# Optimization experiments

Hardware: AMD Instinct MI355X
Metric: run time of the kernel (lower is better)

Reference implementation:

```python
import jax, jax.numpy as jnp
import numpy as np

B, T, V, E = 32, 12, 1024, 64
G = 32           # graph_emb
DAY, WEEK = 288, 7
ALPHA = 0.3      # LeakyReLU slope


def setup_inputs() -> dict:
    key = jax.random.key(0)
    ks = jax.random.split(key, 10)
    return {
        "inputs": jax.random.normal(ks[0], (B, T, V, E), dtype=jnp.float32),
        "n_route": jax.random.randint(ks[1], (B, V), 0, V),
        "s_week": jax.random.randint(ks[2], (B, T), 0, WEEK),
        "s_day": jax.random.randint(ks[3], (B, T), 0, DAY),
        "srpe": jax.random.normal(ks[4], (V, G, E), dtype=jnp.float32) * 0.05,
        "sape": jax.random.normal(ks[5], (V, T, E), dtype=jnp.float32) * 0.05,
        "dow_emb": jax.random.normal(ks[6], (WEEK, V, E), dtype=jnp.float32) * 0.05,
        "tod_emb": jax.random.normal(ks[7], (DAY, V, E), dtype=jnp.float32) * 0.05,
        "connect_weight": jax.random.normal(ks[8], (T, V, 3 * E, E), dtype=jnp.float32) * 0.05,
        "connect_bias": jnp.zeros((T, V, E), dtype=jnp.float32),
    }


def reference(inputs, n_route, s_week, s_day, srpe, sape, dow_emb, tod_emb,
              connect_weight, connect_bias):
    # relation scores: per-channel node-node affinity, relu'd. [V, V, E]
    relation_pos = jnp.einsum('vge,gie->vie', srpe,
                              jnp.transpose(srpe, (1, 0, 2)))
    relation_pos = jax.nn.relu(relation_pos)
    # per-channel graph mixing: contract over source node g. [B, T, V, E]
    x_rel_emb = jnp.einsum('vge,btge->btve', relation_pos, inputs)
    # spatial absolute position embedding gather: [B, V, T, E] -> [B, T, V, E]
    pos_emb = jnp.transpose(sape[n_route], (0, 2, 1, 3))
    # time embeddings: [B, T, V, E]
    time_emb = dow_emb[s_week] + tod_emb[s_day]
    # concat along feature dim -> [B, T, V, 3E]
    x_list = jnp.concatenate([x_rel_emb, pos_emb, time_emb], axis=-1)
    # distinct (3E x E) weight per (timestep, node): batched small matmul
    y = jnp.einsum('btgf,tgfe->btge', x_list, connect_weight) + connect_bias
    return jnp.where(y > 0, y, ALPHA * y)
```

## Files before the change

kernel.cpp:

```cpp
#include <hip/hip_runtime.h>
#include <stdint.h>

#define Bdim 32
#define Tdim 12
#define Vdim 1024
#define Edim 64
#define Gdim 32
#define BT   384

typedef __attribute__((ext_vector_type(8))) short bf16x8;
typedef __attribute__((ext_vector_type(4))) float f32x4;

__device__ __forceinline__ uint pk2(float a, float b) {
    uint r;
    asm("v_cvt_pk_bf16_f32 %0, %1, %2" : "=v"(r) : "v"(a), "v"(b));
    return r;
}
__device__ __forceinline__ ushort f2bf(float f) {
    return (ushort)(pk2(f, f) & 0xffffu);
}

__global__ __launch_bounds__(256) void k_xpose(const float* __restrict__ in,
                                               ushort* __restrict__ Xbf) {
    __shared__ float tile[64][68];
    const int bt = blockIdx.x >> 4;
    const int i0 = (blockIdx.x & 15) << 6;
    const int r  = threadIdx.x >> 2;
    const int q  = threadIdx.x & 3;
    const float* src = in + ((size_t)(bt * Vdim) + i0 + r) * Edim + q * 16;
#pragma unroll
    for (int k = 0; k < 4; ++k)
        *(float4*)&tile[r][q * 16 + 4 * k] = *(const float4*)(src + 4 * k);
    __syncthreads();
    const int e  = r;
    const int ib = q * 16;
    uint4 s0, s1;
    s0.x = pk2(tile[ib + 0][e],  tile[ib + 1][e]);
    s0.y = pk2(tile[ib + 2][e],  tile[ib + 3][e]);
    s0.z = pk2(tile[ib + 4][e],  tile[ib + 5][e]);
    s0.w = pk2(tile[ib + 6][e],  tile[ib + 7][e]);
    s1.x = pk2(tile[ib + 8][e],  tile[ib + 9][e]);
    s1.y = pk2(tile[ib + 10][e], tile[ib + 11][e]);
    s1.z = pk2(tile[ib + 12][e], tile[ib + 13][e]);
    s1.w = pk2(tile[ib + 14][e], tile[ib + 15][e]);
    ushort* dst = Xbf + ((size_t)(e * BT) + bt) * Vdim + i0 + ib;
    *(uint4*)dst = s0;
    *(uint4*)(dst + 8) = s1;
}

__global__ __launch_bounds__(256) void k_se(const float* __restrict__ srpe,
                                            ushort* __restrict__ Se) {
    __shared__ float t2[256][65];
    const int tid = threadIdx.x;
    const int v0 = blockIdx.x * 8;
#pragma unroll
    for (int c = 0; c < 16; ++c) {
        int f = (c * 256 + tid) * 4;
        int vg = f >> 6;
        int e4 = f & 63;
        *(float4*)&t2[vg][e4] = *(const float4*)(srpe + (size_t)v0 * Gdim * Edim + f);
    }
    __syncthreads();
    const int e = tid & 63;
#pragma unroll
    for (int h = 0; h < 2; ++h) {
        const int vv = (tid >> 6) * 2 + h;
        uint4 o[2];
#pragma unroll
        for (int c = 0; c < 2; ++c) {
            o[c].x = pk2(t2[vv * 32 + c * 16 + 0][e],  t2[vv * 32 + c * 16 + 1][e]);
            o[c].y = pk2(t2[vv * 32 + c * 16 + 2][e],  t2[vv * 32 + c * 16 + 3][e]);
            o[c].z = pk2(t2[vv * 32 + c * 16 + 4][e],  t2[vv * 32 + c * 16 + 5][e]);
            o[c].w = pk2(t2[vv * 32 + c * 16 + 6][e],  t2[vv * 32 + c * 16 + 7][e]);
        }
        uint4 o2[2];
#pragma unroll
        for (int c = 0; c < 2; ++c) {
            o2[c].x = pk2(t2[vv * 32 + c * 16 + 8][e],  t2[vv * 32 + c * 16 + 9][e]);
            o2[c].y = pk2(t2[vv * 32 + c * 16 + 10][e], t2[vv * 32 + c * 16 + 11][e]);
            o2[c].z = pk2(t2[vv * 32 + c * 16 + 12][e], t2[vv * 32 + c * 16 + 13][e]);
            o2[c].w = pk2(t2[vv * 32 + c * 16 + 14][e], t2[vv * 32 + c * 16 + 15][e]);
        }
        ushort* dst = Se + ((size_t)(e * Vdim) + v0 + vv) * Gdim;
        *(uint4*)(dst + 0)  = o[0];
        *(uint4*)(dst + 8)  = o2[0];
        *(uint4*)(dst + 16) = o[1];
        *(uint4*)(dst + 24) = o2[1];
    }
}

__global__ __launch_bounds__(256, 2) void k_relmix_mfma(const ushort* __restrict__ Xbf,
                                                        const ushort* __restrict__ Se,
                                                        ushort* __restrict__ xrel) {
    __shared__ __align__(16) ushort A_s[3][192 * 32];
    __shared__ __align__(16) ushort Si_s[3][32 * 32];
    __shared__ __align__(16) ushort R_s[2][128 * 40];

    const int tid = threadIdx.x;
    const int l = tid & 63;
    const int w = tid >> 6;
    const int wm = w >> 1;
    const int wn = w & 1;

    const int raw = blockIdx.x;
    const int wg  = (raw & 7) * 128 + (raw >> 3);
    const int e   = wg >> 4;
    const int btT = (wg >> 3) & 1;
    const int vT  = wg & 7;
    const int bt0 = btT * 192;
    const int v0  = vT * 128;

    const int lr  = l >> 2;
    const int lc  = ((l & 3) ^ (lr & 3)) * 8;

    const ushort* gA  = Xbf + ((size_t)(e * BT + bt0)) * Vdim;
    const ushort* gSi = Se + (size_t)e * Vdim * Gdim;

    bf16x8 svF[2];
    {
        const ushort* gSv = Se + ((size_t)e * Vdim + v0) * Gdim;
#pragma unroll
        for (int k = 0; k < 2; ++k) {
            const int vloc = (2 * w + k) * 16 + (l & 15);
            svF[k] = *(const bf16x8*)(gSv + (size_t)vloc * Gdim + (l >> 4) * 8);
        }
    }
    __builtin_amdgcn_sched_barrier(0);

    if (w < 2)
        __builtin_amdgcn_global_load_lds(gSi + (size_t)(0 + w * 16 + lr) * Gdim + lc,
                                         &Si_s[0][w * 512], 16, 0, 0);
#pragma unroll
    for (int c = 0; c < 3; ++c) {
        int chunk = w * 3 + c;
        __builtin_amdgcn_global_load_lds(gA + (size_t)(chunk * 16 + lr) * Vdim + 0 + lc,
                                         &A_s[0][chunk * 512], 16, 0, 0);
    }
    if (w < 2)
        __builtin_amdgcn_global_load_lds(gSi + (size_t)(32 + w * 16 + lr) * Gdim + lc,
                                         &Si_s[1][w * 512], 16, 0, 0);
#pragma unroll
    for (int c = 0; c < 3; ++c) {
        int chunk = w * 3 + c;
        __builtin_amdgcn_global_load_lds(gA + (size_t)(chunk * 16 + lr) * Vdim + 32 + lc,
                                         &A_s[1][chunk * 512], 16, 0, 0);
    }
    asm volatile("s_waitcnt vmcnt(3)" ::: "memory");
    __builtin_amdgcn_sched_barrier(0);
    __builtin_amdgcn_s_barrier();
    __builtin_amdgcn_sched_barrier(0);

    const f32x4 fz = {0.f, 0.f, 0.f, 0.f};

    auto computeR = [&](int sb, int rb) {
        const int r0 = (l & 15), r1 = 16 + (l & 15);
        const int kg = l >> 4;
        bf16x8 siF0 = *(const bf16x8*)&Si_s[sb][r0 * 32 + (kg ^ (r0 & 3)) * 8];
        bf16x8 siF1 = *(const bf16x8*)&Si_s[sb][r1 * 32 + (kg ^ (r1 & 3)) * 8];
#pragma unroll
        for (int k = 0; k < 2; ++k) {
            const int vloc = (2 * w + k) * 16 + (l & 15);
            f32x4 d0 = __builtin_amdgcn_mfma_f32_16x16x32_bf16(siF0, svF[k], fz, 0, 0, 0);
            f32x4 d1 = __builtin_amdgcn_mfma_f32_16x16x32_bf16(siF1, svF[k], fz, 0, 0, 0);
            uint2 w0, w1;
            w0.x = pk2(fmaxf(d0[0], 0.f), fmaxf(d0[1], 0.f));
            w0.y = pk2(fmaxf(d0[2], 0.f), fmaxf(d0[3], 0.f));
            w1.x = pk2(fmaxf(d1[0], 0.f), fmaxf(d1[1], 0.f));
            w1.y = pk2(fmaxf(d1[2], 0.f), fmaxf(d1[3], 0.f));
            *(uint2*)&R_s[rb][vloc * 40 + kg * 4]      = w0;
            *(uint2*)&R_s[rb][vloc * 40 + 16 + kg * 4] = w1;
        }
    };

    computeR(0, 0);
    asm volatile("s_waitcnt lgkmcnt(0)" ::: "memory");
    __builtin_amdgcn_sched_barrier(0);
    __builtin_amdgcn_s_barrier();
    __builtin_amdgcn_sched_barrier(0);

    f32x4 acc[6][4];
#pragma unroll
    for (int m = 0; m < 6; ++m)
#pragma unroll
        for (int n = 0; n < 4; ++n) acc[m][n] = fz;

    int c0 = 0, c1 = 1, c2 = 2;
    int rc = 0, rn = 1;

    for (int t = 0; t < 32; ++t) {
        const int i0f = ((t + 2) & 31) * 32;
        if (w < 2)
            __builtin_amdgcn_global_load_lds(gSi + (size_t)(i0f + w * 16 + lr) * Gdim + lc,
                                             &Si_s[c2][w * 512], 16, 0, 0);
#pragma unroll
        for (int c = 0; c < 3; ++c) {
            int chunk = w * 3 + c;
            __builtin_amdgcn_global_load_lds(gA + (size_t)(chunk * 16 + lr) * Vdim + i0f + lc,
                                             &A_s[c2][chunk * 512], 16, 0, 0);
        }
        computeR(c1, rn);
        bf16x8 aF[6];
#pragma unroll
        for (int m = 0; m < 6; ++m) {
            const int row = wm * 96 + m * 16 + (l & 15);
            aF[m] = *(const bf16x8*)&A_s[c0][row * 32 + (((l >> 4) ^ (row & 3))) * 8];
        }
        __builtin_amdgcn_s_setprio(1);
#pragma unroll
        for (int n = 0; n < 4; ++n) {
            bf16x8 bF = *(const bf16x8*)&R_s[rc][(wn * 64 + n * 16 + (l & 15)) * 40 + (l >> 4) * 8];
#pragma unroll
            for (int m = 0; m < 6; ++m)
                acc[m][n] = __builtin_amdgcn_mfma_f32_16x16x32_bf16(aF[m], bF, acc[m][n], 0, 0, 0);
        }
        __builtin_amdgcn_s_setprio(0);
        asm volatile("s_waitcnt vmcnt(3) lgkmcnt(0)" ::: "memory");
        __builtin_amdgcn_sched_barrier(0);
        __builtin_amdgcn_s_barrier();
        __builtin_amdgcn_sched_barrier(0);
        int tmp = c0; c0 = c1; c1 = c2; c2 = tmp;
        tmp = rc; rc = rn; rn = tmp;
    }

#pragma unroll
    for (int m = 0; m < 6; ++m) {
        const int btl = bt0 + wm * 96 + m * 16 + (l >> 4) * 4;
#pragma unroll
        for (int j = 0; j < 4; ++j) {
            ushort* row = xrel + ((size_t)(e * BT) + btl + j) * Vdim + v0;
#pragma unroll
            for (int n = 0; n < 4; ++n)
                row[wn * 64 + n * 16 + (l & 15)] = f2bf(acc[m][n][j]);
        }
    }
}

__global__ __launch_bounds__(256) void k_xrelT(const ushort* __restrict__ xr,
                                               ushort* __restrict__ xrT) {
    __shared__ uint t[64 * 256];
    const int tid = threadIdx.x;
    const int bt = blockIdx.x >> 1;
    const int v0 = (blockIdx.x & 1) * 512;
    {
        const int e = tid >> 2, q = tid & 3;
        const ushort* src = xr + ((size_t)(e * BT) + bt) * Vdim + v0 + q * 128;
#pragma unroll
        for (int c = 0; c < 16; ++c) {
            uint4 x = *(const uint4*)(src + c * 8);
            int p = q * 64 + c * 4;
            int sw = ((e & 3) << 3) ^ ((p >> 6) << 2);
            *(uint4*)&t[e * 256 + (p ^ sw)] = x;
        }
    }
    __syncthreads();
    {
        const int p = tid;
        uint lw[32], hw[32];
#pragma unroll
        for (int e2 = 0; e2 < 32; ++e2) {
            const int ea = 2 * e2, eb = 2 * e2 + 1;
            uint xa = t[ea * 256 + (p ^ (((ea & 3) << 3) ^ ((p >> 6) << 2)))];
            uint xb = t[eb * 256 + (p ^ (((eb & 3) << 3) ^ ((p >> 6) << 2)))];
            lw[e2] = (xa & 0xffffu) | (xb << 16);
            hw[e2] = (xa >> 16) | (xb & 0xffff0000u);
        }
        ushort* d0 = xrT + ((size_t)(bt * Vdim) + v0 + 2 * p) * Edim;
        ushort* d1 = d0 + Edim;
#pragma unroll
        for (int c = 0; c < 8; ++c) {
            uint4 o; o.x = lw[c*4]; o.y = lw[c*4+1]; o.z = lw[c*4+2]; o.w = lw[c*4+3];
            *(uint4*)(d0 + c * 8) = o;
        }
#pragma unroll
        for (int c = 0; c < 8; ++c) {
            uint4 o; o.x = hw[c*4]; o.y = hw[c*4+1]; o.z = hw[c*4+2]; o.w = hw[c*4+3];
            *(uint4*)(d1 + c * 8) = o;
        }
    }
}

__global__ __launch_bounds__(256, 4) void k_final(const ushort* __restrict__ xrT,
        const int* __restrict__ n_route, const int* __restrict__ s_week,
        const int* __restrict__ s_day,  const float* __restrict__ sape,
        const float* __restrict__ dow,  const float* __restrict__ tod,
        const float* __restrict__ Wc,   const float* __restrict__ bias,
        float* __restrict__ out) {
    __shared__ __align__(16) uint   Wt[2][64 * 36];
    __shared__ __align__(16) ushort xs[32 * 216];
    __shared__ float bl[64];
    const int tid = threadIdx.x;
    const int l = tid & 63, w = tid >> 6;
    const int v = blockIdx.x & (Vdim - 1);
    const int t = blockIdx.x >> 10;

    const float* Wg = Wc + ((size_t)(t * Vdim + v)) * 192 * Edim;
    const int i16  = tid & 15;
    const int j16  = tid >> 4;
    const int colb = i16 * 4;
    const int swW  = (i16 & 3) << 2;

    float4 wr0[4], wr1[4];
#pragma unroll
    for (int r = 0; r < 4; ++r)
        wr0[r] = *(const float4*)(Wg + (size_t)(j16 * 4 + r) * Edim + colb);
#pragma unroll
    for (int r = 0; r < 4; ++r)
        wr1[r] = *(const float4*)(Wg + (size_t)(64 + j16 * 4 + r) * Edim + colb);

    {
        const int b  = tid >> 3;
        const int e0 = (tid & 7) * 8;
        const int bt = b * Tdim + t;
        uint4 raw = *(const uint4*)(xrT + ((size_t)(bt * Vdim) + v) * Edim + e0);
        *(uint4*)&xs[b * 216 + e0] = raw;
        const int r  = n_route[b * Vdim + v];
        const float* sp = sape + ((size_t)(r * Tdim) + t) * Edim + e0;
        const int wd = s_week[bt], dd = s_day[bt];
        const float* dp = dow + ((size_t)(wd * Vdim) + v) * Edim + e0;
        const float* tp = tod + ((size_t)(dd * Vdim) + v) * Edim + e0;
        uint4 o1, o2;
        o1.x = pk2(sp[0], sp[1]); o1.y = pk2(sp[2], sp[3]);
        o1.z = pk2(sp[4], sp[5]); o1.w = pk2(sp[6], sp[7]);
        *(uint4*)&xs[b * 216 + 64 + e0] = o1;
        o2.x = pk2(dp[0] + tp[0], dp[1] + tp[1]);
        o2.y = pk2(dp[2] + tp[2], dp[3] + tp[3]);
        o2.z = pk2(dp[4] + tp[4], dp[5] + tp[5]);
        o2.w = pk2(dp[6] + tp[6], dp[7] + tp[7]);
        *(uint4*)&xs[b * 216 + 128 + e0] = o2;
    }
    if (tid < 64) bl[tid] = bias[((size_t)(t * Vdim) + v) * Edim + tid];

    auto wwrite = [&](int buf, const float4* wr) {
#pragma unroll
        for (int k = 0; k < 4; ++k) {
            const int e = colb + k;
            uint2 o;
            o.x = pk2(((const float*)&wr[0])[k], ((const float*)&wr[1])[k]);
            o.y = pk2(((const float*)&wr[2])[k], ((const float*)&wr[3])[k]);
            *(uint2*)&Wt[buf][e * 36 + ((2 * j16) ^ swW)] = o;
        }
    };

    const int mt  = w >> 1;
    const int ntb = (w & 1) * 2;
    const f32x4 fz = {0.f, 0.f, 0.f, 0.f};
    f32x4 acc[2] = {fz, fz};
    const int arow = (mt * 16 + (l & 15)) * 216;
    const int g4   = (l >> 4);

    auto computeChunk = [&](int buf, int ksb) {
#pragma unroll
        for (int kk = 0; kk < 2; ++kk) {
            bf16x8 aF = *(const bf16x8*)&xs[arow + (ksb + kk) * 32 + g4 * 8];
#pragma unroll
            for (int ni = 0; ni < 2; ++ni) {
                const int ecol = (ntb + ni) * 16 + (l & 15);
                const int swr  = ((ecol >> 2) & 3) << 2;
                uint4 u = *(const uint4*)&Wt[buf][ecol * 36 + 16 * kk + ((4 * g4) ^ swr)];
                bf16x8 bF;
                __builtin_memcpy(&bF, &u, 16);
                acc[ni] = __builtin_amdgcn_mfma_f32_16x16x32_bf16(aF, bF, acc[ni], 0, 0, 0);
            }
        }
    };

    wwrite(0, wr0);
    __syncthreads();
    float4 wr2[4];
#pragma unroll
    for (int r = 0; r < 4; ++r)
        wr2[r] = *(const float4*)(Wg + (size_t)(128 + j16 * 4 + r) * Edim + colb);
    computeChunk(0, 0);
    wwrite(1, wr1);
    __syncthreads();
    computeChunk(1, 2);
    wwrite(0, wr2);
    __syncthreads();
    computeChunk(0, 4);

    const int brow = mt * 16 + g4 * 4;
#pragma unroll
    for (int ni = 0; ni < 2; ++ni) {
        const int ecol = (ntb + ni) * 16 + (l & 15);
        const float bv = bl[ecol];
#pragma unroll
        for (int j = 0; j < 4; ++j) {
            float s = acc[ni][j] + bv;
            s = s > 0.f ? s : 0.3f * s;
            out[(size_t)(brow + j) * (Tdim * Vdim * Edim)
                + (size_t)t * (Vdim * Edim) + v * Edim + ecol] = s;
        }
    }
}

extern "C" void kernel_launch(void* const* d_in, const int* in_sizes, int n_in,
                              void* d_out, int out_size, void* d_ws, size_t ws_size,
                              hipStream_t stream) {
    const float* inputs = (const float*)d_in[0];
    const int*   n_route= (const int*)d_in[1];
    const int*   s_week = (const int*)d_in[2];
    const int*   s_day  = (const int*)d_in[3];
    const float* srpe   = (const float*)d_in[4];
    const float* sape   = (const float*)d_in[5];
    const float* dow    = (const float*)d_in[6];
    const float* tod    = (const float*)d_in[7];
    const float* Wc     = (const float*)d_in[8];
    const float* bias   = (const float*)d_in[9];

    ushort* Xbf  = (ushort*)d_ws;
    ushort* Se   = (ushort*)((char*)d_ws + (size_t)Edim * BT * Vdim * 2);
    ushort* xrel = (ushort*)d_out;
    ushort* xrT  = (ushort*)d_ws;
    float*  out  = (float*)d_out;

    k_xpose<<<dim3(BT * 16), dim3(256), 0, stream>>>(inputs, Xbf);
    k_se<<<dim3(Vdim / 8), dim3(256), 0, stream>>>(srpe, Se);
    k_relmix_mfma<<<dim3(1024), dim3(256), 0, stream>>>(Xbf, Se, xrel);
    k_xrelT<<<dim3(BT * 2), dim3(256), 0, stream>>>(xrel, xrT);
    k_final<<<dim3(Tdim * Vdim), dim3(256), 0, stream>>>(
        xrT, n_route, s_week, s_day, sape, dow, tod, Wc, bias, out);
}
```

Before: 313.1 us.

## Make k_final persistent over 16 (t,v) tiles with software-pipelined weight prefetch

k_final now launches 768 blocks, and each block walks 16 consecutive (t,v) tiles instead of handling one. Each tile's three 64-row weight chunks are prefetched into registers one chunk ahead across tile boundaries, along with the next tile's activations, embeddings and bias. This overlaps the dominant weight stream with MFMA compute and removes per-block launch and prologue overhead. It uses a third LDS weight buffer, explicit barriers and setprio, and lowers the occupancy target to 3 blocks per CU, which adds register pressure and fewer resident waves.

```diff
diff --git a/kernel.cpp b/kernel.cpp
--- a/kernel.cpp
+++ b/kernel.cpp
@@ -279,116 +279,171 @@
     }
 }
 
-__global__ __launch_bounds__(256, 4) void k_final(const ushort* __restrict__ xrT,
+__global__ __launch_bounds__(256, 3) void k_final(const ushort* __restrict__ xrT,
         const int* __restrict__ n_route, const int* __restrict__ s_week,
         const int* __restrict__ s_day,  const float* __restrict__ sape,
         const float* __restrict__ dow,  const float* __restrict__ tod,
         const float* __restrict__ Wc,   const float* __restrict__ bias,
         float* __restrict__ out) {
-    __shared__ __align__(16) uint   Wt[2][64 * 36];
+    __shared__ __align__(16) uint   Wt[3][64 * 36];
     __shared__ __align__(16) ushort xs[32 * 216];
-    __shared__ float bl[64];
+
     const int tid = threadIdx.x;
     const int l = tid & 63, w = tid >> 6;
-    const int v = blockIdx.x & (Vdim - 1);
-    const int t = blockIdx.x >> 10;
-
-    const float* Wg = Wc + ((size_t)(t * Vdim + v)) * 192 * Edim;
-    const int i16  = tid & 15;
-    const int j16  = tid >> 4;
+    const int mt  = w >> 1;
+    const int ntb = (w & 1) * 2;
+    const int i16 = tid & 15, j16 = tid >> 4;
     const int colb = i16 * 4;
     const int swW  = (i16 & 3) << 2;
-
-    float4 wr0[4], wr1[4];
-#pragma unroll
-    for (int r = 0; r < 4; ++r)
-        wr0[r] = *(const float4*)(Wg + (size_t)(j16 * 4 + r) * Edim + colb);
-#pragma unroll
-    for (int r = 0; r < 4; ++r)
-        wr1[r] = *(const float4*)(Wg + (size_t)(64 + j16 * 4 + r) * Edim + colb);
-
-    {
-        const int b  = tid >> 3;
-        const int e0 = (tid & 7) * 8;
-        const int bt = b * Tdim + t;
-        uint4 raw = *(const uint4*)(xrT + ((size_t)(bt * Vdim) + v) * Edim + e0);
-        *(uint4*)&xs[b * 216 + e0] = raw;
-        const int r  = n_route[b * Vdim + v];
-        const float* sp = sape + ((size_t)(r * Tdim) + t) * Edim + e0;
-        const int wd = s_week[bt], dd = s_day[bt];
-        const float* dp = dow + ((size_t)(wd * Vdim) + v) * Edim + e0;
-        const float* tp = tod + ((size_t)(dd * Vdim) + v) * Edim + e0;
+    const int b8 = tid >> 3, e8 = (tid & 7) * 8;
+    const int g4 = l >> 4;
+    const int ec0 = ntb * 16 + (l & 15), ec1 = ec0 + 16;
+    const int arow = (mt * 16 + (l & 15)) * 216;
+    const f32x4 fz = {0.f, 0.f, 0.f, 0.f};
+
+    const int tau0 = blockIdx.x * 16;
+    const float* Wgb = Wc + (size_t)tau0 * (192 * Edim);
+
+    float4 wr[3][4];
+#pragma unroll
+    for (int c = 0; c < 3; ++c)
+#pragma unroll
+        for (int r = 0; r < 4; ++r)
+            wr[c][r] = *(const float4*)(Wgb + (size_t)c * 4096 + (j16 * 4 + r) * Edim + colb);
+
+    uint4 xrR; float4 spR0, spR1, dpR0, dpR1, tpR0, tpR1;
+    float blc0, blc1, blN0, blN1;
+    int nrN, wdN, ddN;
+
+    {
+        const int t0 = tau0 >> 10, v0_ = tau0 & 1023;
+        const int bt0_ = b8 * Tdim + t0;
+        const int nr0 = n_route[b8 * Vdim + v0_];
+        const int wd0 = s_week[bt0_], dd0 = s_day[bt0_];
+        xrR = *(const uint4*)(xrT + ((size_t)bt0_ * Vdim + v0_) * Edim + e8);
+        const float* sp = sape + ((size_t)nr0 * Tdim + t0) * Edim + e8;
+        spR0 = *(const float4*)sp;       spR1 = *(const float4*)(sp + 4);
+        const float* dp = dow + ((size_t)wd0 * Vdim + v0_) * Edim + e8;
+        dpR0 = *(const float4*)dp;       dpR1 = *(const float4*)(dp + 4);
+        const float* tp = tod + ((size_t)dd0 * Vdim + v0_) * Edim + e8;
+        tpR0 = *(const float4*)tp;       tpR1 = *(const float4*)(tp + 4);
+        blc0 = bias[(size_t)tau0 * Edim + ec0];
+        blc1 = bias[(size_t)tau0 * Edim + ec1];
+    }
+    {
+        *(uint4*)&xs[b8 * 216 + e8] = xrR;
         uint4 o1, o2;
-        o1.x = pk2(sp[0], sp[1]); o1.y = pk2(sp[2], sp[3]);
-        o1.z = pk2(sp[4], sp[5]); o1.w = pk2(sp[6], sp[7]);
-        *(uint4*)&xs[b * 216 + 64 + e0] = o1;
-        o2.x = pk2(dp[0] + tp[0], dp[1] + tp[1]);
-        o2.y = pk2(dp[2] + tp[2], dp[3] + tp[3]);
-        o2.z = pk2(dp[4] + tp[4], dp[5] + tp[5]);
-        o2.w = pk2(dp[6] + tp[6], dp[7] + tp[7]);
-        *(uint4*)&xs[b * 216 + 128 + e0] = o2;
-    }
-    if (tid < 64) bl[tid] = bias[((size_t)(t * Vdim) + v) * Edim + tid];
-
-    auto wwrite = [&](int buf, const float4* wr) {
-#pragma unroll
-        for (int k = 0; k < 4; ++k) {
-            const int e = colb + k;
-            uint2 o;
-            o.x = pk2(((const float*)&wr[0])[k], ((const float*)&wr[1])[k]);
-            o.y = pk2(((const float*)&wr[2])[k], ((const float*)&wr[3])[k]);
-            *(uint2*)&Wt[buf][e * 36 + ((2 * j16) ^ swW)] = o;
-        }
-    };
-
-    const int mt  = w >> 1;
-    const int ntb = (w & 1) * 2;
-    const f32x4 fz = {0.f, 0.f, 0.f, 0.f};
-    f32x4 acc[2] = {fz, fz};
-    const int arow = (mt * 16 + (l & 15)) * 216;
-    const int g4   = (l >> 4);
-
-    auto computeChunk = [&](int buf, int ksb) {
-#pragma unroll
-        for (int kk = 0; kk < 2; ++kk) {
-            bf16x8 aF = *(const bf16x8*)&xs[arow + (ksb + kk) * 32 + g4 * 8];
-#pragma unroll
-            for (int ni = 0; ni < 2; ++ni) {
-                const int ecol = (ntb + ni) * 16 + (l & 15);
-                const int swr  = ((ecol >> 2) & 3) << 2;
-                uint4 u = *(const uint4*)&Wt[buf][ecol * 36 + 16 * kk + ((4 * g4) ^ swr)];
-                bf16x8 bF;
-                __builtin_memcpy(&bF, &u, 16);
-                acc[ni] = __builtin_amdgcn_mfma_f32_16x16x32_bf16(aF, bF, acc[ni], 0, 0, 0);
+        o1.x = pk2(spR0.x, spR0.y); o1.y = pk2(spR0.z, spR0.w);
+        o1.z = pk2(spR1.x, spR1.y); o1.w = pk2(spR1.z, spR1.w);
+        *(uint4*)&xs[b8 * 216 + 64 + e8] = o1;
+        o2.x = pk2(dpR0.x + tpR0.x, dpR0.y + tpR0.y);
+        o2.y = pk2(dpR0.z + tpR0.z, dpR0.w + tpR0.w);
+        o2.z = pk2(dpR1.x + tpR1.x, dpR1.y + tpR1.y);
+        o2.w = pk2(dpR1.z + tpR1.z, dpR1.w + tpR1.w);
+        *(uint4*)&xs[b8 * 216 + 128 + e8] = o2;
+    }
+    {
+        const int tau1 = tau0 + 1;
+        const int t1 = tau1 >> 10, v1 = tau1 & 1023;
+        nrN = n_route[b8 * Vdim + v1];
+        wdN = s_week[b8 * Tdim + t1];
+        ddN = s_day[b8 * Tdim + t1];
+    }
+    __syncthreads();
+
+    for (int k = 0; k < 16; ++k) {
+        const int tau = tau0 + k;
+        const int t_ = tau >> 10, v_ = tau & 1023;
+        f32x4 acc0 = fz, acc1 = fz;
+        bf16x8 aF[6];
+
+#pragma unroll
+        for (int c = 0; c < 3; ++c) {
+#pragma unroll
+            for (int kq = 0; kq < 4; ++kq) {
+                const int e = colb + kq;
+                uint2 o;
+                o.x = pk2(((const float*)&wr[c][0])[kq], ((const float*)&wr[c][1])[kq]);
+                o.y = pk2(((const float*)&wr[c][2])[kq], ((const float*)&wr[c][3])[kq]);
+                *(uint2*)&Wt[c][e * 36 + ((2 * j16) ^ swW)] = o;
             }
-        }
-    };
-
-    wwrite(0, wr0);
-    __syncthreads();
-    float4 wr2[4];
-#pragma unroll
-    for (int r = 0; r < 4; ++r)
-        wr2[r] = *(const float4*)(Wg + (size_t)(128 + j16 * 4 + r) * Edim + colb);
-    computeChunk(0, 0);
-    wwrite(1, wr1);
-    __syncthreads();
-    computeChunk(1, 2);
-    wwrite(0, wr2);
-    __syncthreads();
-    computeChunk(0, 4);
-
-    const int brow = mt * 16 + g4 * 4;
-#pragma unroll
-    for (int ni = 0; ni < 2; ++ni) {
-        const int ecol = (ntb + ni) * 16 + (l & 15);
-        const float bv = bl[ecol];
+            asm volatile("s_waitcnt lgkmcnt(0)" ::: "memory");
+            __builtin_amdgcn_sched_barrier(0);
+            __builtin_amdgcn_s_barrier();
+            __builtin_amdgcn_sched_barrier(0);
+
+            if (c == 0) {
+#pragma unroll
+                for (int ks = 0; ks < 6; ++ks)
+                    aF[ks] = *(const bf16x8*)&xs[arow + ks * 32 + g4 * 8];
+            }
+            if (3 * k + c + 3 < 48) {
+#pragma unroll
+                for (int r = 0; r < 4; ++r)
+                    wr[c][r] = *(const float4*)(Wgb + (size_t)(3 * k + c + 3) * 4096
+                                                + (j16 * 4 + r) * Edim + colb);
+            }
+            if (c == 1 && k < 15) {
+                const int tauN = tau + 1;
+                const int tN = tauN >> 10, vN = tauN & 1023;
+                const int btN = b8 * Tdim + tN;
+                xrR = *(const uint4*)(xrT + ((size_t)btN * Vdim + vN) * Edim + e8);
+                const float* sp = sape + ((size_t)nrN * Tdim + tN) * Edim + e8;
+                spR0 = *(const float4*)sp;       spR1 = *(const float4*)(sp + 4);
+                const float* dp = dow + ((size_t)wdN * Vdim + vN) * Edim + e8;
+                dpR0 = *(const float4*)dp;       dpR1 = *(const float4*)(dp + 4);
+                const float* tp = tod + ((size_t)ddN * Vdim + vN) * Edim + e8;
+                tpR0 = *(const float4*)tp;       tpR1 = *(const float4*)(tp + 4);
+                blN0 = bias[(size_t)tauN * Edim + ec0];
+                blN1 = bias[(size_t)tauN * Edim + ec1];
+                if (k < 14) {
+                    const int tauNN = tau + 2;
+                    const int tNN = tauNN >> 10, vNN = tauNN & 1023;
+                    nrN = n_route[b8 * Vdim + vNN];
+                    wdN = s_week[b8 * Tdim + tNN];
+                    ddN = s_day[b8 * Tdim + tNN];
+                }
+            }
+            __builtin_amdgcn_s_setprio(1);
+#pragma unroll
+            for (int kk = 0; kk < 2; ++kk) {
+                const int ks = c * 2 + kk;
+#pragma unroll
+                for (int ni = 0; ni < 2; ++ni) {
+                    const int ecol = ni ? ec1 : ec0;
+                    const int swr  = ((ecol >> 2) & 3) << 2;
+                    uint4 u = *(const uint4*)&Wt[c][ecol * 36 + 16 * kk + ((4 * g4) ^ swr)];
+                    bf16x8 bF;
+                    __builtin_memcpy(&bF, &u, 16);
+                    if (ni == 0) acc0 = __builtin_amdgcn_mfma_f32_16x16x32_bf16(aF[ks], bF, acc0, 0, 0, 0);
+                    else         acc1 = __builtin_amdgcn_mfma_f32_16x16x32_bf16(aF[ks], bF, acc1, 0, 0, 0);
+                }
+            }
+            __builtin_amdgcn_s_setprio(0);
+        }
+
+        const int brow = mt * 16 + g4 * 4;
 #pragma unroll
         for (int j = 0; j < 4; ++j) {
-            float s = acc[ni][j] + bv;
-            s = s > 0.f ? s : 0.3f * s;
-            out[(size_t)(brow + j) * (Tdim * Vdim * Edim)
-                + (size_t)t * (Vdim * Edim) + v * Edim + ecol] = s;
+            float s0 = acc0[j] + blc0;
+            s0 = s0 > 0.f ? s0 : 0.3f * s0;
+            out[(size_t)((brow + j) * Tdim + t_) * (Vdim * Edim) + v_ * Edim + ec0] = s0;
+            float s1 = acc1[j] + blc1;
+            s1 = s1 > 0.f ? s1 : 0.3f * s1;
+            out[(size_t)((brow + j) * Tdim + t_) * (Vdim * Edim) + v_ * Edim + ec1] = s1;
+        }
+        if (k < 15) {
+            *(uint4*)&xs[b8 * 216 + e8] = xrR;
+            uint4 o1, o2;
+            o1.x = pk2(spR0.x, spR0.y); o1.y = pk2(spR0.z, spR0.w);
+            o1.z = pk2(spR1.x, spR1.y); o1.w = pk2(spR1.z, spR1.w);
+            *(uint4*)&xs[b8 * 216 + 64 + e8] = o1;
+            o2.x = pk2(dpR0.x + tpR0.x, dpR0.y + tpR0.y);
+            o2.y = pk2(dpR0.z + tpR0.z, dpR0.w + tpR0.w);
+            o2.z = pk2(dpR1.x + tpR1.x, dpR1.y + tpR1.y);
+            o2.w = pk2(dpR1.z + tpR1.z, dpR1.w + tpR1.w);
+            *(uint4*)&xs[b8 * 216 + 128 + e8] = o2;
+            blc0 = blN0; blc1 = blN1;
         }
     }
 }
@@ -417,6 +472,6 @@
     k_se<<<dim3(Vdim / 8), dim3(256), 0, stream>>>(srpe, Se);
     k_relmix_mfma<<<dim3(1024), dim3(256), 0, stream>>>(Xbf, Se, xrel);
     k_xrelT<<<dim3(BT * 2), dim3(256), 0, stream>>>(xrel, xrT);
-    k_final<<<dim3(Tdim * Vdim), dim3(256), 0, stream>>>(
+    k_final<<<dim3(768), dim3(256), 0, stream>>>(
         xrT, n_route, s_week, s_day, sape, dow, tod, Wc, bias, out);
 }
```

Result: slower. 320.7 us (+2.4%).

## Drop xrel transpose kernel, gather strided in final kernel, widen LDS swizzle

Applied to the files above, without the earlier changes.

Removes the separate k_xrelT transpose pass. k_final now gathers its eight bf16 x_rel values per thread directly from the E-major xrel layout using strided 2-byte loads, and xrel moves from the output buffer into workspace. This saves a full extra read and write of the intermediate tensor plus one launch. The cost is heavily uncoalesced scattered loads in k_final, which only pay off if neighbouring v blocks hit the same lines in L2. Separately, the LDS XOR swizzle in the relmix kernel adds a second row term to cut bank conflicts on A and Si fragment reads.

```diff
diff --git a/kernel.cpp b/kernel.cpp
--- a/kernel.cpp
+++ b/kernel.cpp
@@ -111,7 +111,7 @@
     const int v0  = vT * 128;
 
     const int lr  = l >> 2;
-    const int lc  = ((l & 3) ^ (lr & 3)) * 8;
+    const int lc  = ((l & 3) ^ (lr & 3) ^ ((lr >> 2) & 3)) * 8;
 
     const ushort* gA  = Xbf + ((size_t)(e * BT + bt0)) * Vdim;
     const ushort* gSi = Se + (size_t)e * Vdim * Gdim;
@@ -155,8 +155,9 @@
     auto computeR = [&](int sb, int rb) {
         const int r0 = (l & 15), r1 = 16 + (l & 15);
         const int kg = l >> 4;
-        bf16x8 siF0 = *(const bf16x8*)&Si_s[sb][r0 * 32 + (kg ^ (r0 & 3)) * 8];
-        bf16x8 siF1 = *(const bf16x8*)&Si_s[sb][r1 * 32 + (kg ^ (r1 & 3)) * 8];
+        const int k0 = (kg ^ (r0 & 3) ^ ((r0 >> 2) & 3)) * 8;
+        bf16x8 siF0 = *(const bf16x8*)&Si_s[sb][r0 * 32 + k0];
+        bf16x8 siF1 = *(const bf16x8*)&Si_s[sb][r1 * 32 + k0];
 #pragma unroll
         for (int k = 0; k < 2; ++k) {
             const int vloc = (2 * w + k) * 16 + (l & 15);
@@ -203,7 +204,8 @@
 #pragma unroll
         for (int m = 0; m < 6; ++m) {
             const int row = wm * 96 + m * 16 + (l & 15);
-            aF[m] = *(const bf16x8*)&A_s[c0][row * 32 + (((l >> 4) ^ (row & 3))) * 8];
+            const int key = ((l >> 4) ^ (row & 3) ^ ((row >> 2) & 3)) * 8;
+            aF[m] = *(const bf16x8*)&A_s[c0][row * 32 + key];
         }
         __builtin_amdgcn_s_setprio(1);
 #pragma unroll
@@ -235,51 +237,7 @@
     }
 }
 
-__global__ __launch_bounds__(256) void k_xrelT(const ushort* __restrict__ xr,
-                                               ushort* __restrict__ xrT) {
-    __shared__ uint t[64 * 256];
-    const int tid = threadIdx.x;
-    const int bt = blockIdx.x >> 1;
-    const int v0 = (blockIdx.x & 1) * 512;
-    {
-        const int e = tid >> 2, q = tid & 3;
-        const ushort* src = xr + ((size_t)(e * BT) + bt) * Vdim + v0 + q * 128;
-#pragma unroll
-        for (int c = 0; c < 16; ++c) {
-            uint4 x = *(const uint4*)(src + c * 8);
-            int p = q * 64 + c * 4;
-            int sw = ((e & 3) << 3) ^ ((p >> 6) << 2);
-            *(uint4*)&t[e * 256 + (p ^ sw)] = x;
-        }
-    }
-    __syncthreads();
-    {
-        const int p = tid;
-        uint lw[32], hw[32];
-#pragma unroll
-        for (int e2 = 0; e2 < 32; ++e2) {
-            const int ea = 2 * e2, eb = 2 * e2 + 1;
-            uint xa = t[ea * 256 + (p ^ (((ea & 3) << 3) ^ ((p >> 6) << 2)))];
-            uint xb = t[eb * 256 + (p ^ (((eb & 3) << 3) ^ ((p >> 6) << 2)))];
-            lw[e2] = (xa & 0xffffu) | (xb << 16);
-            hw[e2] = (xa >> 16) | (xb & 0xffff0000u);
-        }
-        ushort* d0 = xrT + ((size_t)(bt * Vdim) + v0 + 2 * p) * Edim;
-        ushort* d1 = d0 + Edim;
-#pragma unroll
-        for (int c = 0; c < 8; ++c) {
-            uint4 o; o.x = lw[c*4]; o.y = lw[c*4+1]; o.z = lw[c*4+2]; o.w = lw[c*4+3];
-            *(uint4*)(d0 + c * 8) = o;
-        }
-#pragma unroll
-        for (int c = 0; c < 8; ++c) {
-            uint4 o; o.x = hw[c*4]; o.y = hw[c*4+1]; o.z = hw[c*4+2]; o.w = hw[c*4+3];
-            *(uint4*)(d1 + c * 8) = o;
-        }
-    }
-}
-
-__global__ __launch_bounds__(256, 4) void k_final(const ushort* __restrict__ xrT,
+__global__ __launch_bounds__(256, 4) void k_final(const ushort* __restrict__ xrel,
         const int* __restrict__ n_route, const int* __restrict__ s_week,
         const int* __restrict__ s_day,  const float* __restrict__ sape,
         const float* __restrict__ dow,  const float* __restrict__ tod,
@@ -311,8 +269,16 @@
         const int b  = tid >> 3;
         const int e0 = (tid & 7) * 8;
         const int bt = b * Tdim + t;
-        uint4 raw = *(const uint4*)(xrT + ((size_t)(bt * Vdim) + v) * Edim + e0);
-        *(uint4*)&xs[b * 216 + e0] = raw;
+        ushort tmp[8];
+#pragma unroll
+        for (int k = 0; k < 8; ++k)
+            tmp[k] = xrel[((size_t)((e0 + k) * BT) + bt) * Vdim + v];
+        uint4 o0;
+        o0.x = (uint)tmp[0] | ((uint)tmp[1] << 16);
+        o0.y = (uint)tmp[2] | ((uint)tmp[3] << 16);
+        o0.z = (uint)tmp[4] | ((uint)tmp[5] << 16);
+        o0.w = (uint)tmp[6] | ((uint)tmp[7] << 16);
+        *(uint4*)&xs[b * 216 + e0] = o0;
         const int r  = n_route[b * Vdim + v];
         const float* sp = sape + ((size_t)(r * Tdim) + t) * Edim + e0;
         const int wd = s_week[bt], dd = s_day[bt];
@@ -409,14 +375,12 @@
 
     ushort* Xbf  = (ushort*)d_ws;
     ushort* Se   = (ushort*)((char*)d_ws + (size_t)Edim * BT * Vdim * 2);
-    ushort* xrel = (ushort*)d_out;
-    ushort* xrT  = (ushort*)d_ws;
+    ushort* xrel = (ushort*)((char*)d_ws + (size_t)64 * 1024 * 1024);
     float*  out  = (float*)d_out;
 
     k_xpose<<<dim3(BT * 16), dim3(256), 0, stream>>>(inputs, Xbf);
     k_se<<<dim3(Vdim / 8), dim3(256), 0, stream>>>(srpe, Se);
     k_relmix_mfma<<<dim3(1024), dim3(256), 0, stream>>>(Xbf, Se, xrel);
-    k_xrelT<<<dim3(BT * 2), dim3(256), 0, stream>>>(xrel, xrT);
     k_final<<<dim3(Tdim * Vdim), dim3(256), 0, stream>>>(
-        xrT, n_route, s_week, s_day, sape, dow, tod, Wc, bias, out);
-}
+        xrel, n_route, s_week, s_day, sape, dow, tod, Wc, bias, out);
+}
```

After: 346.2 us. 1.11x slower.
